# Optimization experiments

Hardware: AMD Instinct MI355X
Metric: run time of the kernel (lower is better)

## Reference

```python
import jax, jax.numpy as jnp
import numpy as np

B, LC, LQ, D = 16, 2048, 1024, 512


def setup_inputs() -> dict:
    key = jax.random.key(0)
    k1, k2, k3 = jax.random.split(key, 3)
    context = jax.random.normal(k1, (B, LC, D), dtype=jnp.float32)
    query = jax.random.normal(k2, (LQ, D), dtype=jnp.float32)
    # nn.Linear(3*D, 1, bias=False).weight  -> [1, 3D]
    w = jax.random.normal(k3, (1, 3 * D), dtype=jnp.float32) * (1.0 / np.sqrt(3 * D))
    return {"context": context, "query": query, "w": w}


def reference(context, query, w):
    # context: [B, Lc, D], query: [Lq, D], w: [1, 3D]
    d = context.shape[-1]
    wc, wq, wm = w[0, :d], w[0, d:2 * d], w[0, 2 * d:]
    # S[b,i,j] = <context[b,i], wc> + <query[j], wq> + <context[b,i]*wm, query[j]>
    # (algebraic collapse of Linear(cat(c, q, c*q)) -- identical math, no 4D tensor)
    S = ((context @ wc)[:, :, None]
         + (query @ wq)[None, None, :]
         + jnp.einsum('bid,jd->bij', context * wm, query))  # [B, Lc, Lq]
    # softmax over context dim (dim=1), then permute -> A[b,j,i]
    A = jnp.transpose(jax.nn.softmax(S, axis=1), (0, 2, 1))  # [B, Lq, Lc]
    # query mask: sign(|sum_d query|), same for every batch element
    qmask = jnp.sign(jnp.abs(jnp.sum(query, axis=-1)))  # [Lq]
    A = A * qmask[None, :, None]
    # attd[b,j,i,d] = A[b,j,i] * context[b,i,d]
    # G_att[b,i,d] = context[b,i,d] * sum_j A[b,j,i]
    colsum = jnp.sum(A, axis=1)  # [B, Lc]
    G_att = context * colsum[:, :, None]  # [B, Lc, D]
    # H[b,j,d] = sum_i A[b,j,i] * context[b,i,d]
    H = jnp.einsum('bji,bid->bjd', A, context)  # [B, Lq, D]
    G = jnp.concatenate((context, G_att), axis=2)  # [B, Lc, 2D]
    return (G, H)
```

## Files before the change

### kernel.cpp

```cpp
#include <hip/hip_runtime.h>
#include <stdint.h>

#define BB 16
#define LC 2048
#define LQ 1024
#define DD 512

typedef _Float16 f16x8 __attribute__((ext_vector_type(8)));
typedef _Float16 f16x4 __attribute__((ext_vector_type(4)));
typedef float f32x4 __attribute__((ext_vector_type(4)));

#define MFMA16 __builtin_amdgcn_mfma_f32_16x16x32_f16

__device__ __forceinline__ void async16(_Float16* lds, const _Float16* g) {
    __builtin_amdgcn_global_load_lds(
        (const __attribute__((address_space(1))) void*)g,
        (__attribute__((address_space(3))) void*)lds, 16, 0, 0);
}

__global__ void zero_k(float* __restrict__ p, int n) {
    int i = blockIdx.x * blockDim.x + threadIdx.x;
    if (i < n) p[i] = 0.0f;
}

__global__ __launch_bounds__(256) void prep_ctx(
    const float* __restrict__ ctx, const float* __restrict__ w,
    _Float16* __restrict__ cm, _Float16* __restrict__ ct, float* __restrict__ cb)
{
    __shared__ _Float16 sm[64][68];
    const int b = blockIdx.z;
    const int i0 = blockIdx.y * 64;
    const int d0 = blockIdx.x * 64;
    const int t = threadIdx.x;
    const int tx = t & 15, ty = t >> 4;
    const float* wc = w;
    const float* wm = w + 2 * DD;
    const float4 wc4 = *(const float4*)(wc + d0 + tx * 4);
    const float4 wm4 = *(const float4*)(wm + d0 + tx * 4);
    for (int k = 0; k < 4; ++k) {
        const int r = ty + 16 * k;
        const int ig = i0 + r;
        const float4 v = *(const float4*)(ctx + ((size_t)(b * LC + ig)) * DD + d0 + tx * 4);
        f16x4 cmv = { (_Float16)(v.x * wm4.x), (_Float16)(v.y * wm4.y),
                      (_Float16)(v.z * wm4.z), (_Float16)(v.w * wm4.w) };
        *(f16x4*)(cm + ((size_t)(b * LC + ig)) * DD + d0 + tx * 4) = cmv;
        sm[tx * 4 + 0][r] = (_Float16)v.x;
        sm[tx * 4 + 1][r] = (_Float16)v.y;
        sm[tx * 4 + 2][r] = (_Float16)v.z;
        sm[tx * 4 + 3][r] = (_Float16)v.w;
        float p = v.x * wc4.x + v.y * wc4.y + v.z * wc4.z + v.w * wc4.w;
        p += __shfl_xor(p, 1); p += __shfl_xor(p, 2);
        p += __shfl_xor(p, 4); p += __shfl_xor(p, 8);
        if (tx == 0) atomicAdd(&cb[b * LC + ig], p);
    }
    __syncthreads();
    for (int k = 0; k < 4; ++k) {
        const int dd = ty + 16 * k;
        f16x4 o = *(const f16x4*)(&sm[dd][tx * 4]);
        *(f16x4*)(ct + ((size_t)(b * DD + d0 + dd)) * LC + i0 + tx * 4) = o;
    }
}

__global__ __launch_bounds__(128) void prep_q(
    const float* __restrict__ q, _Float16* __restrict__ qh, float* __restrict__ qmask)
{
    const int j = blockIdx.x;
    const int t = threadIdx.x;
    const float4 v = *(const float4*)(q + (size_t)j * DD + t * 4);
    f16x4 qv = { (_Float16)v.x, (_Float16)v.y, (_Float16)v.z, (_Float16)v.w };
    *(f16x4*)(qh + (size_t)j * DD + t * 4) = qv;
    float sq = v.x + v.y + v.z + v.w;
    for (int m = 1; m < 64; m <<= 1) sq += __shfl_xor(sq, m);
    __shared__ float ss[2];
    if ((t & 63) == 0) ss[t >> 6] = sq;
    __syncthreads();
    if (t == 0) qmask[j] = ((ss[0] + ss[1]) != 0.0f) ? 1.0f : 0.0f;
}

__global__ __launch_bounds__(256) void gemm1(
    const _Float16* __restrict__ qh, const _Float16* __restrict__ cm,
    const float* __restrict__ cb,
    _Float16* __restrict__ E, float* __restrict__ lsum)
{
    __shared__ __align__(16) _Float16 smA[128 * 32];
    __shared__ __align__(16) _Float16 smB[128 * 32];
    int orig = blockIdx.x + 16 * (blockIdx.y + 8 * blockIdx.z);
    int wg = (orig & 7) * (2048 >> 3) + (orig >> 3);
    const int m0 = (wg & 15) * 128;
    const int n0 = ((wg >> 4) & 7) * 128;
    const int b  = wg >> 7;
    const int t = threadIdx.x;
    const int lane = t & 63;
    const int wid = t >> 6;
    const int wvm = wid >> 1, wvn = wid & 1;
    const int li = lane & 15, lg = lane >> 4;
    f32x4 acc[4][4] = {};
    const int srow = lane >> 2;
    const int scol = (lane & 3) * 8;
    const _Float16* gA0 = cm + ((size_t)(b * LC + m0 + wid * 32 + srow)) * DD + scol;
    const _Float16* gA1 = gA0 + (size_t)16 * DD;
    const _Float16* gB0 = qh + (size_t)(n0 + wid * 32 + srow) * DD + scol;
    const _Float16* gB1 = gB0 + (size_t)16 * DD;
    _Float16* sA0 = smA + wid * 32 * 32;
    _Float16* sA1 = sA0 + 16 * 32;
    _Float16* sB0 = smB + wid * 32 * 32;
    _Float16* sB1 = sB0 + 16 * 32;
    for (int ks = 0; ks < DD; ks += 32) {
        __syncthreads();
        async16(sA0, gA0 + ks);
        async16(sA1, gA1 + ks);
        async16(sB0, gB0 + ks);
        async16(sB1, gB1 + ks);
        __syncthreads();
        f16x8 af[4], bf[4];
        #pragma unroll
        for (int mt = 0; mt < 4; ++mt)
            af[mt] = *(const f16x8*)(smA + (wvm * 64 + mt * 16 + li) * 32 + lg * 8);
        #pragma unroll
        for (int nt = 0; nt < 4; ++nt)
            bf[nt] = *(const f16x8*)(smB + (wvn * 64 + nt * 16 + li) * 32 + lg * 8);
        #pragma unroll
        for (int mt = 0; mt < 4; ++mt)
            #pragma unroll
            for (int nt = 0; nt < 4; ++nt)
                acc[mt][nt] = MFMA16(af[mt], bf[nt], acc[mt][nt], 0, 0, 0);
    }
    __syncthreads();
    float* rs = (float*)smA;
    if (t < 128) rs[t] = 0.0f;
    __syncthreads();
    f32x4 cb4[4];
    #pragma unroll
    for (int mt = 0; mt < 4; ++mt)
        cb4[mt] = *(const f32x4*)(cb + b * LC + m0 + wvm * 64 + mt * 16 + lg * 4);
    #pragma unroll
    for (int nt = 0; nt < 4; ++nt) {
        const int jl = wvn * 64 + nt * 16 + li;
        const int j = n0 + jl;
        _Float16* Ej = E + ((size_t)(b * LQ + j)) * LC + m0 + wvm * 64;
        float rsv = 0.0f;
        #pragma unroll
        for (int mt = 0; mt < 4; ++mt) {
            f16x4 ev;
            #pragma unroll
            for (int r = 0; r < 4; ++r) {
                float e = __expf(acc[mt][nt][r] + cb4[mt][r]);
                rsv += e;
                ev[r] = (_Float16)e;
            }
            *(f16x4*)(Ej + mt * 16 + lg * 4) = ev;
        }
        rsv += __shfl_xor(rsv, 16);
        rsv += __shfl_xor(rsv, 32);
        if (lg == 0) atomicAdd(&rs[jl], rsv);
    }
    __syncthreads();
    if (t < 128) atomicAdd(&lsum[b * LQ + n0 + t], rs[t]);
}

__global__ __launch_bounds__(256) void gemm2(
    const _Float16* __restrict__ E, const _Float16* __restrict__ ct,
    const float* __restrict__ lsum, const float* __restrict__ qmask,
    float* __restrict__ H)
{
    __shared__ __align__(16) _Float16 smA[128 * 32];
    __shared__ __align__(16) _Float16 smB[128 * 32];
    int orig = blockIdx.x + 4 * (blockIdx.y + 8 * blockIdx.z);
    int wg = (orig & 7) * (512 >> 3) + (orig >> 3);
    const int m0 = (wg & 3) * 128;
    const int n0 = ((wg >> 2) & 7) * 128;
    const int b  = wg >> 5;
    const int t = threadIdx.x;
    const int lane = t & 63;
    const int wid = t >> 6;
    const int wvm = wid >> 1, wvn = wid & 1;
    const int li = lane & 15, lg = lane >> 4;
    f32x4 acc[4][4] = {};
    const int srow = lane >> 2;
    const int scol = (lane & 3) * 8;
    const _Float16* gA0 = ct + ((size_t)(b * DD + m0 + wid * 32 + srow)) * LC + scol;
    const _Float16* gA1 = gA0 + (size_t)16 * LC;
    const _Float16* gB0 = E + ((size_t)(b * LQ + n0 + wid * 32 + srow)) * LC + scol;
    const _Float16* gB1 = gB0 + (size_t)16 * LC;
    _Float16* sA0 = smA + wid * 32 * 32;
    _Float16* sA1 = sA0 + 16 * 32;
    _Float16* sB0 = smB + wid * 32 * 32;
    _Float16* sB1 = sB0 + 16 * 32;
    for (int ks = 0; ks < LC; ks += 32) {
        __syncthreads();
        async16(sA0, gA0 + ks);
        async16(sA1, gA1 + ks);
        async16(sB0, gB0 + ks);
        async16(sB1, gB1 + ks);
        __syncthreads();
        f16x8 af[4], bf[4];
        #pragma unroll
        for (int mt = 0; mt < 4; ++mt)
            af[mt] = *(const f16x8*)(smA + (wvm * 64 + mt * 16 + li) * 32 + lg * 8);
        #pragma unroll
        for (int nt = 0; nt < 4; ++nt)
            bf[nt] = *(const f16x8*)(smB + (wvn * 64 + nt * 16 + li) * 32 + lg * 8);
        #pragma unroll
        for (int mt = 0; mt < 4; ++mt)
            #pragma unroll
            for (int nt = 0; nt < 4; ++nt)
                acc[mt][nt] = MFMA16(af[mt], bf[nt], acc[mt][nt], 0, 0, 0);
    }
    #pragma unroll
    for (int nt = 0; nt < 4; ++nt) {
        const int j = n0 + wvn * 64 + nt * 16 + li;
        const float s = qmask[j] / lsum[b * LQ + j];
        float* Hj = H + ((size_t)(b * LQ + j)) * DD + m0 + wvm * 64;
        #pragma unroll
        for (int mt = 0; mt < 4; ++mt) {
            f32x4 o = acc[mt][nt] * s;
            *(f32x4*)(Hj + mt * 16 + lg * 4) = o;
        }
    }
}

__global__ __launch_bounds__(256) void colsum_k(
    const _Float16* __restrict__ E, const float* __restrict__ lsum,
    const float* __restrict__ qmask, float* __restrict__ cs)
{
    __shared__ float sscale[LQ];
    __shared__ float red[16][132];
    const int b = blockIdx.y;
    const int i0 = blockIdx.x * 128;
    const int t = threadIdx.x;
    for (int j = t; j < LQ; j += 256) sscale[j] = qmask[j] / lsum[b * LQ + j];
    __syncthreads();
    const int iw = t & 15;
    const int jg = t >> 4;
    const _Float16* Eb = E + ((size_t)(b * LQ + jg * 64)) * LC + i0 + iw * 8;
    float acc[8] = {};
    #pragma unroll 4
    for (int k = 0; k < 64; ++k) {
        f16x8 v = *(const f16x8*)(Eb + (size_t)k * LC);
        const float s = sscale[jg * 64 + k];
        #pragma unroll
        for (int q = 0; q < 8; ++q) acc[q] += s * (float)v[q];
    }
    #pragma unroll
    for (int q = 0; q < 8; ++q) red[jg][iw * 8 + q] = acc[q];
    __syncthreads();
    if (t < 128) {
        float s = 0.0f;
        #pragma unroll
        for (int g = 0; g < 16; ++g) s += red[g][t];
        cs[b * LC + i0 + t] = s;
    }
}

__global__ __launch_bounds__(128) void gwrite(
    const float* __restrict__ ctx, const float* __restrict__ cs, float* __restrict__ G)
{
    const int b = blockIdx.y, i = blockIdx.x, t = threadIdx.x;
    const float c = cs[b * LC + i];
    const size_t ro = (size_t)(b * LC + i);
    const float4 v = *(const float4*)(ctx + ro * DD + t * 4);
    float4 u; u.x = v.x * c; u.y = v.y * c; u.z = v.z * c; u.w = v.w * c;
    *(float4*)(G + ro * (2 * DD) + t * 4) = v;
    *(float4*)(G + ro * (2 * DD) + DD + t * 4) = u;
}

extern "C" void kernel_launch(void* const* d_in, const int* in_sizes, int n_in,
                              void* d_out, int out_size, void* d_ws, size_t ws_size,
                              hipStream_t stream)
{
    (void)in_sizes; (void)n_in; (void)out_size; (void)ws_size;
    const float* ctx = (const float*)d_in[0];
    const float* qry = (const float*)d_in[1];
    const float* w   = (const float*)d_in[2];
    float* G = (float*)d_out;
    float* H = G + (size_t)BB * LC * (2 * DD);

    char* ws = (char*)d_ws;
    _Float16* E  = (_Float16*)ws;
    _Float16* cm = (_Float16*)(ws + ((size_t)64 << 20));
    _Float16* ct = (_Float16*)(ws + ((size_t)96 << 20));
    _Float16* qh = (_Float16*)(ws + ((size_t)128 << 20));
    float* stats = (float*)(ws + ((size_t)130 << 20));
    float* cb    = stats;
    float* lsum  = cb + BB * LC;
    float* cs    = lsum + BB * LQ;
    float* qmask = cs + BB * LC;

    const int nzero = BB * LC + BB * LQ;
    zero_k<<<dim3((nzero + 255) / 256), 256, 0, stream>>>(stats, nzero);
    prep_ctx<<<dim3(DD / 64, LC / 64, BB), 256, 0, stream>>>(ctx, w, cm, ct, cb);
    prep_q<<<dim3(LQ), 128, 0, stream>>>(qry, qh, qmask);
    gemm1<<<dim3(LC / 128, LQ / 128, BB), 256, 0, stream>>>(qh, cm, cb, E, lsum);
    gemm2<<<dim3(DD / 128, LQ / 128, BB), 256, 0, stream>>>(E, ct, lsum, qmask, H);
    colsum_k<<<dim3(LC / 128, BB), 256, 0, stream>>>(E, lsum, qmask, cs);
    gwrite<<<dim3(LC, BB), 128, 0, stream>>>(ctx, cs, G);
}
```

Baseline: 357.5 us.

## Rewrite both GEMMs with larger tiles, double-buffered async LDS loads and swizzle

Both GEMM kernels move to 512-thread workgroups with larger output tiles (256x256 for gemm1, 128x256 for gemm2). They now use double-buffered global-to-LDS async loads paced by explicit vmcnt waits and raw s_barriers instead of two __syncthreads per k-step. An XOR swizzle on the LDS k-offset is added to avoid bank conflicts, and MFMA blocks are interleaved with LDS reads under s_setprio. The aim is to hide global load latency and improve operand reuse. The cost is higher register pressure (up to 128 accumulator floats in gemm1) and far fewer workgroups (512 and 256), which may underfill the 256 CUs for gemm2.

```diff
diff --git a/kernel.cpp b/kernel.cpp
--- a/kernel.cpp
+++ b/kernel.cpp
@@ -11,6 +11,10 @@
 typedef float f32x4 __attribute__((ext_vector_type(4)));
 
 #define MFMA16 __builtin_amdgcn_mfma_f32_16x16x32_f16
+#define BARM()   asm volatile("s_barrier" ::: "memory")
+#define VMCNT0() asm volatile("s_waitcnt vmcnt(0)" ::: "memory")
+#define VMCNT3() asm volatile("s_waitcnt vmcnt(3)" ::: "memory")
+#define VMCNT4() asm volatile("s_waitcnt vmcnt(4)" ::: "memory")
 
 __device__ __forceinline__ void async16(_Float16* lds, const _Float16* g) {
     __builtin_amdgcn_global_load_lds(
@@ -77,144 +81,216 @@
     if (t == 0) qmask[j] = ((ss[0] + ss[1]) != 0.0f) ? 1.0f : 0.0f;
 }
 
-__global__ __launch_bounds__(256) void gemm1(
+__global__ __launch_bounds__(512, 1) void gemm1(
     const _Float16* __restrict__ qh, const _Float16* __restrict__ cm,
     const float* __restrict__ cb,
     _Float16* __restrict__ E, float* __restrict__ lsum)
 {
-    __shared__ __align__(16) _Float16 smA[128 * 32];
-    __shared__ __align__(16) _Float16 smB[128 * 32];
-    int orig = blockIdx.x + 16 * (blockIdx.y + 8 * blockIdx.z);
-    int wg = (orig & 7) * (2048 >> 3) + (orig >> 3);
-    const int m0 = (wg & 15) * 128;
-    const int n0 = ((wg >> 4) & 7) * 128;
-    const int b  = wg >> 7;
+    __shared__ __align__(16) _Float16 As[2][256 * 32];
+    __shared__ __align__(16) _Float16 Bs[2][256 * 32];
+    const int orig = blockIdx.x;
+    const int wg = (orig & 7) * 64 + (orig >> 3);
+    const int b  = wg >> 5;
+    const int m0 = ((wg >> 2) & 7) * 256;
+    const int n0 = (wg & 3) * 256;
     const int t = threadIdx.x;
     const int lane = t & 63;
-    const int wid = t >> 6;
-    const int wvm = wid >> 1, wvn = wid & 1;
+    const int w = t >> 6;
+    const int wvm = w >> 2, wvn = w & 3;
     const int li = lane & 15, lg = lane >> 4;
-    f32x4 acc[4][4] = {};
-    const int srow = lane >> 2;
-    const int scol = (lane & 3) * 8;
-    const _Float16* gA0 = cm + ((size_t)(b * LC + m0 + wid * 32 + srow)) * DD + scol;
+
+    const int swz = (((lane & 3) ^ ((lane >> 3) & 3)) * 8);
+    const int rA = w * 32 + (lane >> 2);
+    const _Float16* gA0 = cm + ((size_t)(b * LC + m0 + rA)) * DD + swz;
     const _Float16* gA1 = gA0 + (size_t)16 * DD;
-    const _Float16* gB0 = qh + (size_t)(n0 + wid * 32 + srow) * DD + scol;
+    const _Float16* gB0 = qh + (size_t)(n0 + rA) * DD + swz;
     const _Float16* gB1 = gB0 + (size_t)16 * DD;
-    _Float16* sA0 = smA + wid * 32 * 32;
-    _Float16* sA1 = sA0 + 16 * 32;
-    _Float16* sB0 = smB + wid * 32 * 32;
-    _Float16* sB1 = sB0 + 16 * 32;
-    for (int ks = 0; ks < DD; ks += 32) {
-        __syncthreads();
-        async16(sA0, gA0 + ks);
-        async16(sA1, gA1 + ks);
-        async16(sB0, gB0 + ks);
-        async16(sB1, gB1 + ks);
-        __syncthreads();
+
+    const int kc = ((lg ^ ((li >> 1) & 3)) * 8);
+    const int raA = (wvm * 128 + li) * 32 + kc;
+    const int raB = (wvn * 64 + li) * 32 + kc;
+
+    f32x4 acc[8][4] = {};
+
+#define G1_STAGE(p, ks) do { \
+    async16(&As[p][w * 32 * 32],           gA0 + (ks)); \
+    async16(&As[p][w * 32 * 32 + 16 * 32], gA1 + (ks)); \
+    async16(&Bs[p][w * 32 * 32],           gB0 + (ks)); \
+    async16(&Bs[p][w * 32 * 32 + 16 * 32], gB1 + (ks)); } while (0)
+
+    G1_STAGE(0, 0);
+    G1_STAGE(1, 32);
+
+    #pragma unroll 2
+    for (int kt = 0; kt < 16; ++kt) {
+        const int p = kt & 1;
+        const _Float16* A  = As[p];
+        const _Float16* Bt = Bs[p];
+        if (kt == 15) { VMCNT0(); } else { VMCNT4(); }
+        BARM();
         f16x8 af[4], bf[4];
         #pragma unroll
-        for (int mt = 0; mt < 4; ++mt)
-            af[mt] = *(const f16x8*)(smA + (wvm * 64 + mt * 16 + li) * 32 + lg * 8);
-        #pragma unroll
-        for (int nt = 0; nt < 4; ++nt)
-            bf[nt] = *(const f16x8*)(smB + (wvn * 64 + nt * 16 + li) * 32 + lg * 8);
-        #pragma unroll
-        for (int mt = 0; mt < 4; ++mt)
-            #pragma unroll
-            for (int nt = 0; nt < 4; ++nt)
-                acc[mt][nt] = MFMA16(af[mt], bf[nt], acc[mt][nt], 0, 0, 0);
-    }
-    __syncthreads();
-    float* rs = (float*)smA;
-    if (t < 128) rs[t] = 0.0f;
-    __syncthreads();
-    f32x4 cb4[4];
+        for (int m = 0; m < 4; ++m) af[m] = *(const f16x8*)(A + raA + m * 16 * 32);
+        bf[0] = *(const f16x8*)(Bt + raB);
+        bf[1] = *(const f16x8*)(Bt + raB + 16 * 32);
+        BARM();
+        __builtin_amdgcn_s_setprio(1);
+        #pragma unroll
+        for (int m = 0; m < 4; ++m) {
+            acc[m][0] = MFMA16(af[m], bf[0], acc[m][0], 0, 0, 0);
+            acc[m][1] = MFMA16(af[m], bf[1], acc[m][1], 0, 0, 0);
+        }
+        __builtin_amdgcn_s_setprio(0);
+        BARM();
+        bf[2] = *(const f16x8*)(Bt + raB + 2 * 16 * 32);
+        bf[3] = *(const f16x8*)(Bt + raB + 3 * 16 * 32);
+        BARM();
+        __builtin_amdgcn_s_setprio(1);
+        #pragma unroll
+        for (int m = 0; m < 4; ++m) {
+            acc[m][2] = MFMA16(af[m], bf[2], acc[m][2], 0, 0, 0);
+            acc[m][3] = MFMA16(af[m], bf[3], acc[m][3], 0, 0, 0);
+        }
+        __builtin_amdgcn_s_setprio(0);
+        BARM();
+        #pragma unroll
+        for (int m = 0; m < 4; ++m) af[m] = *(const f16x8*)(A + raA + (4 + m) * 16 * 32);
+        BARM();
+        __builtin_amdgcn_s_setprio(1);
+        #pragma unroll
+        for (int m = 0; m < 4; ++m) {
+            acc[4 + m][2] = MFMA16(af[m], bf[2], acc[4 + m][2], 0, 0, 0);
+            acc[4 + m][3] = MFMA16(af[m], bf[3], acc[4 + m][3], 0, 0, 0);
+        }
+        __builtin_amdgcn_s_setprio(0);
+        BARM();
+        __builtin_amdgcn_sched_barrier(0);
+        if (kt < 14) G1_STAGE(p, (kt + 2) * 32);
+        __builtin_amdgcn_s_setprio(1);
+        #pragma unroll
+        for (int m = 0; m < 4; ++m) {
+            acc[4 + m][0] = MFMA16(af[m], bf[0], acc[4 + m][0], 0, 0, 0);
+            acc[4 + m][1] = MFMA16(af[m], bf[1], acc[4 + m][1], 0, 0, 0);
+        }
+        __builtin_amdgcn_s_setprio(0);
+    }
+
+    float* rs = (float*)&As[0][0];
+    if (t < 256) rs[t] = 0.0f;
+    __syncthreads();
+    f32x4 cbv[8];
     #pragma unroll
-    for (int mt = 0; mt < 4; ++mt)
-        cb4[mt] = *(const f32x4*)(cb + b * LC + m0 + wvm * 64 + mt * 16 + lg * 4);
+    for (int m = 0; m < 8; ++m)
+        cbv[m] = *(const f32x4*)(cb + b * LC + m0 + wvm * 128 + m * 16 + lg * 4);
     #pragma unroll
-    for (int nt = 0; nt < 4; ++nt) {
-        const int jl = wvn * 64 + nt * 16 + li;
+    for (int nf = 0; nf < 4; ++nf) {
+        const int jl = wvn * 64 + nf * 16 + li;
         const int j = n0 + jl;
-        _Float16* Ej = E + ((size_t)(b * LQ + j)) * LC + m0 + wvm * 64;
+        _Float16* Ej = E + ((size_t)(b * LQ + j)) * LC + m0 + wvm * 128;
         float rsv = 0.0f;
         #pragma unroll
-        for (int mt = 0; mt < 4; ++mt) {
+        for (int m = 0; m < 8; ++m) {
             f16x4 ev;
             #pragma unroll
             for (int r = 0; r < 4; ++r) {
-                float e = __expf(acc[mt][nt][r] + cb4[mt][r]);
+                float e = __expf(acc[m][nf][r] + cbv[m][r]);
                 rsv += e;
                 ev[r] = (_Float16)e;
             }
-            *(f16x4*)(Ej + mt * 16 + lg * 4) = ev;
+            *(f16x4*)(Ej + m * 16 + lg * 4) = ev;
         }
         rsv += __shfl_xor(rsv, 16);
         rsv += __shfl_xor(rsv, 32);
         if (lg == 0) atomicAdd(&rs[jl], rsv);
     }
     __syncthreads();
-    if (t < 128) atomicAdd(&lsum[b * LQ + n0 + t], rs[t]);
-}
-
-__global__ __launch_bounds__(256) void gemm2(
+    if (t < 256) atomicAdd(&lsum[b * LQ + n0 + t], rs[t]);
+}
+
+__global__ __launch_bounds__(512, 1) void gemm2(
     const _Float16* __restrict__ E, const _Float16* __restrict__ ct,
     const float* __restrict__ lsum, const float* __restrict__ qmask,
     float* __restrict__ H)
 {
-    __shared__ __align__(16) _Float16 smA[128 * 32];
-    __shared__ __align__(16) _Float16 smB[128 * 32];
-    int orig = blockIdx.x + 4 * (blockIdx.y + 8 * blockIdx.z);
-    int wg = (orig & 7) * (512 >> 3) + (orig >> 3);
-    const int m0 = (wg & 3) * 128;
-    const int n0 = ((wg >> 2) & 7) * 128;
-    const int b  = wg >> 5;
+    __shared__ __align__(16) _Float16 Ad[2][128 * 32];
+    __shared__ __align__(16) _Float16 Bd[2][256 * 32];
+    const int orig = blockIdx.x;
+    const int wg = (orig & 7) * 32 + (orig >> 3);
+    const int b  = wg >> 4;
+    const int m0 = ((wg >> 2) & 3) * 128;
+    const int n0 = (wg & 3) * 256;
     const int t = threadIdx.x;
     const int lane = t & 63;
-    const int wid = t >> 6;
-    const int wvm = wid >> 1, wvn = wid & 1;
+    const int w = t >> 6;
+    const int wvm = w >> 2, wvn = w & 3;
     const int li = lane & 15, lg = lane >> 4;
+
+    const int swz = (((lane & 3) ^ ((lane >> 3) & 3)) * 8);
+    const int rA = w * 16 + (lane >> 2);
+    const _Float16* gA = ct + ((size_t)(b * DD + m0 + rA)) * LC + swz;
+    const int rB = w * 32 + (lane >> 2);
+    const _Float16* gB0 = E + ((size_t)(b * LQ + n0 + rB)) * LC + swz;
+    const _Float16* gB1 = gB0 + (size_t)16 * LC;
+
+    const int kc = ((lg ^ ((li >> 1) & 3)) * 8);
+    const int raA = (wvm * 64 + li) * 32 + kc;
+    const int raB = (wvn * 64 + li) * 32 + kc;
+
     f32x4 acc[4][4] = {};
-    const int srow = lane >> 2;
-    const int scol = (lane & 3) * 8;
-    const _Float16* gA0 = ct + ((size_t)(b * DD + m0 + wid * 32 + srow)) * LC + scol;
-    const _Float16* gA1 = gA0 + (size_t)16 * LC;
-    const _Float16* gB0 = E + ((size_t)(b * LQ + n0 + wid * 32 + srow)) * LC + scol;
-    const _Float16* gB1 = gB0 + (size_t)16 * LC;
-    _Float16* sA0 = smA + wid * 32 * 32;
-    _Float16* sA1 = sA0 + 16 * 32;
-    _Float16* sB0 = smB + wid * 32 * 32;
-    _Float16* sB1 = sB0 + 16 * 32;
-    for (int ks = 0; ks < LC; ks += 32) {
-        __syncthreads();
-        async16(sA0, gA0 + ks);
-        async16(sA1, gA1 + ks);
-        async16(sB0, gB0 + ks);
-        async16(sB1, gB1 + ks);
-        __syncthreads();
+
+#define G2_STAGE(p, ks) do { \
+    async16(&Ad[p][w * 16 * 32],           gA  + (ks)); \
+    async16(&Bd[p][w * 32 * 32],           gB0 + (ks)); \
+    async16(&Bd[p][w * 32 * 32 + 16 * 32], gB1 + (ks)); } while (0)
+
+    G2_STAGE(0, 0);
+    G2_STAGE(1, 32);
+
+    #pragma unroll 2
+    for (int kt = 0; kt < 64; ++kt) {
+        const int p = kt & 1;
+        const _Float16* A  = Ad[p];
+        const _Float16* Bt = Bd[p];
+        if (kt == 63) { VMCNT0(); } else { VMCNT3(); }
+        BARM();
         f16x8 af[4], bf[4];
         #pragma unroll
-        for (int mt = 0; mt < 4; ++mt)
-            af[mt] = *(const f16x8*)(smA + (wvm * 64 + mt * 16 + li) * 32 + lg * 8);
-        #pragma unroll
-        for (int nt = 0; nt < 4; ++nt)
-            bf[nt] = *(const f16x8*)(smB + (wvn * 64 + nt * 16 + li) * 32 + lg * 8);
-        #pragma unroll
-        for (int mt = 0; mt < 4; ++mt)
-            #pragma unroll
-            for (int nt = 0; nt < 4; ++nt)
-                acc[mt][nt] = MFMA16(af[mt], bf[nt], acc[mt][nt], 0, 0, 0);
-    }
+        for (int m = 0; m < 4; ++m) af[m] = *(const f16x8*)(A + raA + m * 16 * 32);
+        bf[0] = *(const f16x8*)(Bt + raB);
+        bf[1] = *(const f16x8*)(Bt + raB + 16 * 32);
+        BARM();
+        __builtin_amdgcn_s_setprio(1);
+        #pragma unroll
+        for (int m = 0; m < 4; ++m) {
+            acc[m][0] = MFMA16(af[m], bf[0], acc[m][0], 0, 0, 0);
+            acc[m][1] = MFMA16(af[m], bf[1], acc[m][1], 0, 0, 0);
+        }
+        __builtin_amdgcn_s_setprio(0);
+        BARM();
+        bf[2] = *(const f16x8*)(Bt + raB + 2 * 16 * 32);
+        bf[3] = *(const f16x8*)(Bt + raB + 3 * 16 * 32);
+        BARM();
+        __builtin_amdgcn_s_setprio(1);
+        #pragma unroll
+        for (int m = 0; m < 4; ++m) {
+            acc[m][2] = MFMA16(af[m], bf[2], acc[m][2], 0, 0, 0);
+            acc[m][3] = MFMA16(af[m], bf[3], acc[m][3], 0, 0, 0);
+        }
+        __builtin_amdgcn_s_setprio(0);
+        BARM();
+        __builtin_amdgcn_sched_barrier(0);
+        if (kt < 62) G2_STAGE(p, (kt + 2) * 32);
+    }
+
     #pragma unroll
-    for (int nt = 0; nt < 4; ++nt) {
-        const int j = n0 + wvn * 64 + nt * 16 + li;
+    for (int nf = 0; nf < 4; ++nf) {
+        const int j = n0 + wvn * 64 + nf * 16 + li;
         const float s = qmask[j] / lsum[b * LQ + j];
         float* Hj = H + ((size_t)(b * LQ + j)) * DD + m0 + wvm * 64;
         #pragma unroll
-        for (int mt = 0; mt < 4; ++mt) {
-            f32x4 o = acc[mt][nt] * s;
-            *(f32x4*)(Hj + mt * 16 + lg * 4) = o;
+        for (int m = 0; m < 4; ++m) {
+            f32x4 o = acc[m][nf] * s;
+            *(f32x4*)(Hj + m * 16 + lg * 4) = o;
         }
     }
 }
@@ -290,8 +366,8 @@
     zero_k<<<dim3((nzero + 255) / 256), 256, 0, stream>>>(stats, nzero);
     prep_ctx<<<dim3(DD / 64, LC / 64, BB), 256, 0, stream>>>(ctx, w, cm, ct, cb);
     prep_q<<<dim3(LQ), 128, 0, stream>>>(qry, qh, qmask);
-    gemm1<<<dim3(LC / 128, LQ / 128, BB), 256, 0, stream>>>(qh, cm, cb, E, lsum);
-    gemm2<<<dim3(DD / 128, LQ / 128, BB), 256, 0, stream>>>(E, ct, lsum, qmask, H);
+    gemm1<<<dim3(512), 512, 0, stream>>>(qh, cm, cb, E, lsum);
+    gemm2<<<dim3(256), 512, 0, stream>>>(E, ct, lsum, qmask, H);
     colsum_k<<<dim3(LC / 128, BB), 256, 0, stream>>>(E, lsum, qmask, cs);
     gwrite<<<dim3(LC, BB), 128, 0, stream>>>(ctx, cs, G);
 }
```

Result: slower. 368.5 us (+3.1%).
